# Kernel optimization log

Measured on AMD Instinct MI355X. Metric: run time of the kernel, lower is better.

Reference implementation:

```python
import jax, jax.numpy as jnp
import numpy as np

N_USERS = 1_000_000
N_PRODUCTS = 500_000
N_CATEGORIES = 1_000
F = 64          # n_factors
L = 2           # n_layers
B = 16384       # batch
K = 50          # max neighbors (padded)


def setup_inputs() -> dict:
    key = jax.random.key(0)
    ks = jax.random.split(key, 12)
    return {
        "user_idx": jax.random.randint(ks[0], (B,), 0, N_USERS),
        "product_idx": jax.random.randint(ks[1], (B,), 0, N_PRODUCTS),
        "category_idx": jax.random.randint(ks[2], (B,), 0, N_CATEGORIES),
        "neighbor_idx": jax.random.randint(ks[3], (B, K), 0, N_USERS),
        "neighbor_lens": jax.random.randint(ks[4], (B,), 0, K + 1),
        # learned parameters (init mimics the torch module: std=0.01 embeds)
        "user_emb": 0.01 * jax.random.normal(ks[5], (N_USERS, F), dtype=jnp.float32),
        "product_emb": 0.01 * jax.random.normal(ks[6], (N_PRODUCTS, F), dtype=jnp.float32),
        "category_emb": 0.01 * jax.random.normal(ks[7], (N_CATEGORIES, F), dtype=jnp.float32),
        "user_bias_tab": 0.01 * jax.random.normal(ks[8], (N_USERS,), dtype=jnp.float32),
        "product_bias_tab": 0.01 * jax.random.normal(ks[9], (N_PRODUCTS,), dtype=jnp.float32),
        "global_bias": jnp.zeros((), dtype=jnp.float32),
        "W": 0.1 * jax.random.normal(ks[10], (L, F, F), dtype=jnp.float32),  # diffusion Linear weights
        "b": jnp.zeros((L, F), dtype=jnp.float32),                           # diffusion Linear biases
    }


def reference(user_idx, product_idx, category_idx, neighbor_idx, neighbor_lens,
              user_emb, product_emb, category_emb, user_bias_tab,
              product_bias_tab, global_bias, W, b):
    # --- social diffusion ---
    u = user_emb[user_idx]                                  # [B, F]
    nbr = user_emb[neighbor_idx]                            # [B, K, F]
    mask = (jnp.arange(K)[None, :] < neighbor_lens[:, None]).astype(u.dtype)  # [B, K]
    cnt = mask.sum(axis=1, keepdims=True)                   # [B, 1]
    # masked mean of neighbor embeddings (same each layer in the original)
    nbr_mean = (nbr * mask[:, :, None]).sum(axis=1) / jnp.maximum(cnt, 1.0)  # [B, F]
    has_nbr = (neighbor_lens > 0)[:, None]                  # [B, 1]
    for l in range(L):
        transformed = jax.nn.relu((u + nbr_mean) @ W[l].T + b[l])
        u = jnp.where(has_nbr, transformed, u)              # empty-neighbor rows pass through
    # --- prediction ---
    combined_prod = product_emb[product_idx] + 0.3 * category_emb[category_idx]  # [B, F]
    interaction = jnp.sum(u * combined_prod, axis=1)        # [B]
    return global_bias + user_bias_tab[user_idx] + product_bias_tab[product_idx] + interaction
```

## Files before the change

kernel.cpp:

```cpp
#include <hip/hip_runtime.h>


#define RPW 4
#define WPB 4
#define WSTR 68

static __device__ __forceinline__ float readlane_f(float v, int l) {
    return __uint_as_float((unsigned)__builtin_amdgcn_readlane(__float_as_uint(v), l));
}

__global__ __launch_bounds__(256, 4)
void diffnet_fwd(const int* __restrict__ user_idx,
                 const int* __restrict__ product_idx,
                 const int* __restrict__ category_idx,
                 const int* __restrict__ neighbor_idx,
                 const int* __restrict__ neighbor_lens,
                 const float* __restrict__ user_emb,
                 const float* __restrict__ product_emb,
                 const float* __restrict__ category_emb,
                 const float* __restrict__ user_bias,
                 const float* __restrict__ product_bias,
                 const float* __restrict__ global_bias,
                 const float* __restrict__ W,
                 const float* __restrict__ bvec,
                 float* __restrict__ out)
{
    __shared__ float Wlds[128 * WSTR];

    const int tid  = threadIdx.x;
    const int lane = tid & 63;
    const int wid  = tid >> 6;

    #pragma unroll
    for (int it = 0; it < 8; ++it) {
        const int g   = it * 256 + tid;
        const int row = g >> 4;
        const int jg  = g & 15;
        const float4 w4 = reinterpret_cast<const float4*>(W)[g];
        *reinterpret_cast<float4*>(&Wlds[row * WSTR + jg * 4]) = w4;
    }
    __syncthreads();

    const int wave_gid = blockIdx.x * WPB + wid;
    const int row0 = wave_gid * RPW;

    const float gb = global_bias[0];
    const float b0 = bvec[lane];
    const float b1 = bvec[64 + lane];

    float u[RPW], m[RPW], comb[RPW], bias[RPW];
    int   lens[RPW];

    #pragma unroll
    for (int r = 0; r < RPW; ++r) {
        const int row = __builtin_amdgcn_readfirstlane(row0 + r);
        const int uid = user_idx[row];
        const int pid = product_idx[row];
        const int cid = category_idx[row];
        const int len = neighbor_lens[row];
        lens[r] = len;

        u[r]    = user_emb[(size_t)uid * 64 + lane];
        comb[r] = product_emb[(size_t)pid * 64 + lane]
                + 0.3f * category_emb[(size_t)cid * 64 + lane];
        bias[r] = gb + user_bias[uid] + product_bias[pid];

        const int* nptr = neighbor_idx + (size_t)row * 50;
        float nsum = 0.f;
        const int g8 = len >> 3;
        for (int g = 0; g < g8; ++g) {
            const int kb = g * 8;
            float a[8];
            #pragma unroll
            for (int i = 0; i < 8; ++i) {
                const int n = nptr[kb + i];
                a[i] = user_emb[(size_t)n * 64 + lane];
            }
            nsum += ((a[0] + a[1]) + (a[2] + a[3]))
                  + ((a[4] + a[5]) + (a[6] + a[7]));
        }
        const int kb = g8 * 8;
        if (kb < len) {
            float a[8];
            #pragma unroll
            for (int i = 0; i < 8; ++i) {
                const int kk = kb + i;
                const int kc = (kk < len) ? kk : (len - 1);
                const int n  = nptr[kc];
                const float v = user_emb[(size_t)n * 64 + lane];
                a[i] = (kk < len) ? v : 0.f;
            }
            nsum += ((a[0] + a[1]) + (a[2] + a[3]))
                  + ((a[4] + a[5]) + (a[6] + a[7]));
        }
        const float cnt = (float)(len > 0 ? len : 1);
        m[r] = nsum / cnt;
    }

    float x[RPW], acc[RPW];
    #pragma unroll
    for (int l = 0; l < 2; ++l) {
        #pragma unroll
        for (int r = 0; r < RPW; ++r) {
            x[r]   = u[r] + m[r];
            acc[r] = (l == 0) ? b0 : b1;
        }
        const float* wbase = &Wlds[(l * 64 + lane) * WSTR];
        #pragma unroll
        for (int jg = 0; jg < 16; ++jg) {
            const float4 w4 = *reinterpret_cast<const float4*>(wbase + jg * 4);
            float wv[4];
            wv[0] = w4.x; wv[1] = w4.y; wv[2] = w4.z; wv[3] = w4.w;
            #pragma unroll
            for (int i = 0; i < 4; ++i) {
                const int j = jg * 4 + i;
                #pragma unroll
                for (int r = 0; r < RPW; ++r) {
                    acc[r] = fmaf(readlane_f(x[r], j), wv[i], acc[r]);
                }
            }
        }
        #pragma unroll
        for (int r = 0; r < RPW; ++r)
            if (lens[r] > 0) u[r] = fmaxf(acc[r], 0.f);
    }

    #pragma unroll
    for (int r = 0; r < RPW; ++r) {
        float v = u[r] * comb[r];
        #pragma unroll
        for (int off = 32; off > 0; off >>= 1)
            v += __shfl_xor(v, off, 64);
        if (lane == 0) out[row0 + r] = bias[r] + v;
    }
}

extern "C" void kernel_launch(void* const* d_in, const int* in_sizes, int n_in,
                              void* d_out, int out_size, void* d_ws, size_t ws_size,
                              hipStream_t stream) {
    const int*   user_idx      = (const int*)  d_in[0];
    const int*   product_idx   = (const int*)  d_in[1];
    const int*   category_idx  = (const int*)  d_in[2];
    const int*   neighbor_idx  = (const int*)  d_in[3];
    const int*   neighbor_lens = (const int*)  d_in[4];
    const float* user_emb      = (const float*)d_in[5];
    const float* product_emb   = (const float*)d_in[6];
    const float* category_emb  = (const float*)d_in[7];
    const float* user_bias     = (const float*)d_in[8];
    const float* product_bias  = (const float*)d_in[9];
    const float* global_bias   = (const float*)d_in[10];
    const float* W             = (const float*)d_in[11];
    const float* bvec          = (const float*)d_in[12];
    float* out = (float*)d_out;

    diffnet_fwd<<<1024, 256, 0, stream>>>(
        user_idx, product_idx, category_idx, neighbor_idx, neighbor_lens,
        user_emb, product_emb, category_emb, user_bias, product_bias,
        global_bias, W, bvec, out);
}
```

Before: 398.0 us.

## Halve rows per wave, transpose W in LDS, fully unroll neighbor gather

Rows per wave drop from 4 to 2 and the grid doubles to 2048 blocks, so more waves are in flight to hide latency on the memory-bound neighbor gathers. W is stored transposed in LDS with stride 65, so each lane reads one conflict-free scalar per j instead of a float4 row. All row metadata is loaded up front, and the neighbor gather becomes a fully unrolled 6x8+2 loop with masked clamped loads. In exchange, each block repeats the 32 KB W staging twice as often, and the fixed unrolled loop increases register pressure.

After: 395.9 us. Within noise of the previous version (-0.5%).

```diff
diff --git a/kernel.cpp b/kernel.cpp
--- a/kernel.cpp
+++ b/kernel.cpp
@@ -1,9 +1,10 @@
 #include <hip/hip_runtime.h>
 
 
-#define RPW 4
-#define WPB 4
-#define WSTR 68
+#define WPB  4
+#define RPW  2
+#define WSTR 65
+#define KMAX 50
 
 static __device__ __forceinline__ float readlane_f(float v, int l) {
     return __uint_as_float((unsigned)__builtin_amdgcn_readlane(__float_as_uint(v), l));
@@ -25,113 +26,115 @@
                  const float* __restrict__ bvec,
                  float* __restrict__ out)
 {
-    __shared__ float Wlds[128 * WSTR];
+    __shared__ float WT[2 * 64 * WSTR];
 
     const int tid  = threadIdx.x;
     const int lane = tid & 63;
-    const int wid  = tid >> 6;
 
     #pragma unroll
     for (int it = 0; it < 8; ++it) {
-        const int g   = it * 256 + tid;
-        const int row = g >> 4;
-        const int jg  = g & 15;
+        const int g  = it * 256 + tid;
         const float4 w4 = reinterpret_cast<const float4*>(W)[g];
-        *reinterpret_cast<float4*>(&Wlds[row * WSTR + jg * 4]) = w4;
+        const int fr = g >> 4;
+        const int jg = g & 15;
+        const int l  = fr >> 6;
+        const int f  = fr & 63;
+        float* base = &WT[l * 64 * WSTR + f];
+        base[(4 * jg + 0) * WSTR] = w4.x;
+        base[(4 * jg + 1) * WSTR] = w4.y;
+        base[(4 * jg + 2) * WSTR] = w4.z;
+        base[(4 * jg + 3) * WSTR] = w4.w;
     }
     __syncthreads();
 
-    const int wave_gid = blockIdx.x * WPB + wid;
-    const int row0 = wave_gid * RPW;
+    const int wid  = tid >> 6;
+    const int row0 = (blockIdx.x * WPB + wid) * RPW;
 
+    int rows[RPW], lens[RPW], uids[RPW], pids[RPW], cids[RPW];
+    #pragma unroll
+    for (int r = 0; r < RPW; ++r) {
+        const int row = __builtin_amdgcn_readfirstlane(row0 + r);
+        rows[r] = row;
+        lens[r] = neighbor_lens[row];
+        uids[r] = user_idx[row];
+        pids[r] = product_idx[row];
+        cids[r] = category_idx[row];
+    }
     const float gb = global_bias[0];
-    const float b0 = bvec[lane];
-    const float b1 = bvec[64 + lane];
 
-    float u[RPW], m[RPW], comb[RPW], bias[RPW];
-    int   lens[RPW];
+    float u[RPW], comb[RPW], bias[RPW], m[RPW];
+    #pragma unroll
+    for (int r = 0; r < RPW; ++r) {
+        u[r]    = user_emb[((size_t)uids[r] << 6) + lane];
+        comb[r] = product_emb[((size_t)pids[r] << 6) + lane]
+                + 0.3f * category_emb[((size_t)cids[r] << 6) + lane];
+        bias[r] = gb + user_bias[uids[r]] + product_bias[pids[r]];
+    }
 
     #pragma unroll
     for (int r = 0; r < RPW; ++r) {
-        const int row = __builtin_amdgcn_readfirstlane(row0 + r);
-        const int uid = user_idx[row];
-        const int pid = product_idx[row];
-        const int cid = category_idx[row];
-        const int len = neighbor_lens[row];
-        lens[r] = len;
-
-        u[r]    = user_emb[(size_t)uid * 64 + lane];
-        comb[r] = product_emb[(size_t)pid * 64 + lane]
-                + 0.3f * category_emb[(size_t)cid * 64 + lane];
-        bias[r] = gb + user_bias[uid] + product_bias[pid];
-
-        const int* nptr = neighbor_idx + (size_t)row * 50;
+        const int len = lens[r];
         float nsum = 0.f;
-        const int g8 = len >> 3;
-        for (int g = 0; g < g8; ++g) {
-            const int kb = g * 8;
-            float a[8];
+        if (len > 0) {
+            const int* nbase = neighbor_idx + rows[r] * KMAX;
+            const int  last  = nbase[len - 1];
+            float tsum = 0.f;
             #pragma unroll
-            for (int i = 0; i < 8; ++i) {
-                const int n = nptr[kb + i];
-                a[i] = user_emb[(size_t)n * 64 + lane];
+            for (int g = 0; g < 6; ++g) {
+                if (len > g * 8) {
+                    float a[8];
+                    #pragma unroll
+                    for (int i = 0; i < 8; ++i) {
+                        const int kk = g * 8 + i;
+                        const int n0 = nbase[kk];
+                        const int n  = (kk < len) ? n0 : last;
+                        const float v = user_emb[((size_t)n << 6) + lane];
+                        a[i] = (kk < len) ? v : 0.f;
+                    }
+                    tsum += ((a[0] + a[1]) + (a[2] + a[3]))
+                          + ((a[4] + a[5]) + (a[6] + a[7]));
+                }
             }
-            nsum += ((a[0] + a[1]) + (a[2] + a[3]))
-                  + ((a[4] + a[5]) + (a[6] + a[7]));
+            if (len > 48) {
+                const int n0 = nbase[48];
+                const int n1 = nbase[49];
+                const int nb = (49 < len) ? n1 : last;
+                const float va = user_emb[((size_t)n0 << 6) + lane];
+                float       vb = user_emb[((size_t)nb << 6) + lane];
+                vb = (49 < len) ? vb : 0.f;
+                tsum += va + vb;
+            }
+            nsum = tsum / (float)len;
         }
-        const int kb = g8 * 8;
-        if (kb < len) {
-            float a[8];
-            #pragma unroll
-            for (int i = 0; i < 8; ++i) {
-                const int kk = kb + i;
-                const int kc = (kk < len) ? kk : (len - 1);
-                const int n  = nptr[kc];
-                const float v = user_emb[(size_t)n * 64 + lane];
-                a[i] = (kk < len) ? v : 0.f;
-            }
-            nsum += ((a[0] + a[1]) + (a[2] + a[3]))
-                  + ((a[4] + a[5]) + (a[6] + a[7]));
-        }
-        const float cnt = (float)(len > 0 ? len : 1);
-        m[r] = nsum / cnt;
+        m[r] = nsum;
     }
 
-    float x[RPW], acc[RPW];
+    const float bl0 = bvec[lane];
+    const float bl1 = bvec[64 + lane];
     #pragma unroll
     for (int l = 0; l < 2; ++l) {
+        const float x0 = u[0] + m[0];
+        const float x1 = u[1] + m[1];
+        float acc0 = l ? bl1 : bl0;
+        float acc1 = acc0;
+        const float* wt = &WT[l * 64 * WSTR + lane];
         #pragma unroll
-        for (int r = 0; r < RPW; ++r) {
-            x[r]   = u[r] + m[r];
-            acc[r] = (l == 0) ? b0 : b1;
+        for (int j = 0; j < 64; ++j) {
+            const float wv = wt[j * WSTR];
+            acc0 = fmaf(readlane_f(x0, j), wv, acc0);
+            acc1 = fmaf(readlane_f(x1, j), wv, acc1);
         }
-        const float* wbase = &Wlds[(l * 64 + lane) * WSTR];
-        #pragma unroll
-        for (int jg = 0; jg < 16; ++jg) {
-            const float4 w4 = *reinterpret_cast<const float4*>(wbase + jg * 4);
-            float wv[4];
-            wv[0] = w4.x; wv[1] = w4.y; wv[2] = w4.z; wv[3] = w4.w;
-            #pragma unroll
-            for (int i = 0; i < 4; ++i) {
-                const int j = jg * 4 + i;
-                #pragma unroll
-                for (int r = 0; r < RPW; ++r) {
-                    acc[r] = fmaf(readlane_f(x[r], j), wv[i], acc[r]);
-                }
-            }
-        }
-        #pragma unroll
-        for (int r = 0; r < RPW; ++r)
-            if (lens[r] > 0) u[r] = fmaxf(acc[r], 0.f);
+        if (lens[0] > 0) u[0] = fmaxf(acc0, 0.f);
+        if (lens[1] > 0) u[1] = fmaxf(acc1, 0.f);
     }
 
     #pragma unroll
     for (int r = 0; r < RPW; ++r) {
         float v = u[r] * comb[r];
         #pragma unroll
-        for (int off = 32; off > 0; off >>= 1)
+        for (int off = 32; off; off >>= 1)
             v += __shfl_xor(v, off, 64);
-        if (lane == 0) out[row0 + r] = bias[r] + v;
+        if (lane == 0) out[rows[r]] = bias[r] + v;
     }
 }
 
@@ -153,7 +156,7 @@
     const float* bvec          = (const float*)d_in[12];
     float* out = (float*)d_out;
 
-    diffnet_fwd<<<1024, 256, 0, stream>>>(
+    diffnet_fwd<<<2048, 256, 0, stream>>>(
         user_idx, product_idx, category_idx, neighbor_idx, neighbor_lens,
         user_emb, product_emb, category_emb, user_bias, product_bias,
         global_bias, W, bvec, out);
```
